# Kernel optimization log

Hardware: AMD Instinct MI355X
Metric: run time of the kernel (lower is better)

## Reference

```python
import jax, jax.numpy as jnp
import numpy as np
from jax.scipy.special import logsumexp

EPS = 0.1
MAX_ITER = 10


def setup_inputs() -> dict:
    key = jax.random.key(0)
    kx, ky, kp, kq = jax.random.split(key, 4)
    N, M, D = 4096, 4096, 64
    x = jax.random.normal(kx, (N, D), dtype=jnp.float32)
    y = jax.random.normal(ky, (M, D), dtype=jnp.float32)
    p = jax.random.uniform(kp, (N,), dtype=jnp.float32, minval=0.1, maxval=1.0)
    q = jax.random.uniform(kq, (M,), dtype=jnp.float32, minval=0.1, maxval=1.0)
    p = p / p.sum()  # valid probability marginals (log(p) is taken)
    q = q / q.sum()
    return {"x": x, "y": y, "p": p, "q": q}


def _cost_matrix(x, y):
    # squared L2 cost: C[i,j] = ||x_i - y_j||^2, shape [N, M]
    return jnp.sum((x[:, None, :] - y[None, :, :]) ** 2, axis=-1)


def _S(C, f, g):
    # eq. 4.43/4.44 log-domain kernel: (-C + f_i + g_j) / eps
    return (-C + f[:, None] + g[None, :]) / EPS


def _sinkhorn(C, p, q):
    logp = jnp.log(p)
    logq = jnp.log(q)
    f0 = jnp.zeros_like(p)
    g0 = jnpep = jnp.zeros_like(q)

    def step(carry, _):
        f, g = carry
        f = f + EPS * (logp - logsumexp(_S(C, f, g), axis=-1))   # row reduce
        g = g + EPS * (logq - logsumexp(_S(C, f, g), axis=0))    # col reduce (== .T row reduce)
        return (f, g), None

    (f, g), _ = jax.lax.scan(step, (f0, jnp.zeros_like(q)), None, length=MAX_ITER)
    P = jnp.exp(_S(C, f, g))
    w_cost = jnp.sum(P * C)
    return w_cost, P


def reference(x, y, p, q):
    C = _cost_matrix(x, y)
    return _sinkhorn(C, p, q)
```

## Files before the change

### kernel.cpp

```cpp
#include <hip/hip_runtime.h>
#include <hip/hip_bf16.h>
#include <cstdint>
#include <cstddef>

#define NROW 4096
#define NM ((size_t)NROW * (size_t)NROW)

#define SCONST 14.426950408889634f
#define EPS_LN2 0.0693147180559945f
#define ENC 461.66241308446827f
#define DEC 0.0625f
#define NEGBIG -3.0e38f

#if __has_builtin(__builtin_amdgcn_exp2f)
#define FEXP2(x) __builtin_amdgcn_exp2f(x)
#else
#define FEXP2(x) exp2f(x)
#endif
#if __has_builtin(__builtin_amdgcn_logf)
#define FLOG2(x) __builtin_amdgcn_logf(x)
#else
#define FLOG2(x) log2f(x)
#endif

__global__ void init_kernel(const float* __restrict__ x, const float* __restrict__ y,
                            const float* __restrict__ p, const float* __restrict__ q,
                            float* __restrict__ lp, float* __restrict__ lq,
                            float* __restrict__ a,
                            float* __restrict__ xn, float* __restrict__ yn) {
    int t = blockIdx.x * blockDim.x + threadIdx.x;
    if (t >= NROW) return;
    lp[t] = FLOG2(p[t]);
    lq[t] = FLOG2(q[t]);
    const float* xr = x + (size_t)t * 64;
    const float* yr = y + (size_t)t * 64;
    float sx = 0.f, sy = 0.f;
    #pragma unroll
    for (int d = 0; d < 64; ++d) {
        sx = fmaf(xr[d], xr[d], sx);
        sy = fmaf(yr[d], yr[d], sy);
    }
    xn[t] = sx; yn[t] = sy;
    a[t] = -SCONST * sy;
}

__global__ __launch_bounds__(256) void M16_kernel(const float* __restrict__ x,
                                                  const float* __restrict__ y,
                                                  int16_t* __restrict__ M16) {
    __shared__ float xs[64 * 65];
    __shared__ float ys[64 * 65];
    int tid = threadIdx.x;
    int it = blockIdx.y, jt = blockIdx.x;
    for (int k = tid; k < 4096; k += 256) {
        int r = k >> 6, d = k & 63;
        xs[r * 65 + d] = x[(size_t)it * 4096 + k];
        ys[r * 65 + d] = y[(size_t)jt * 4096 + k];
    }
    __syncthreads();
    int rl = tid >> 4;
    int cl = tid & 15;
    float acc[4][4] = {};
    #pragma unroll 8
    for (int d = 0; d < 64; ++d) {
        float xv[4], yv[4];
        #pragma unroll
        for (int i = 0; i < 4; ++i) xv[i] = xs[(rl + 16 * i) * 65 + d];
        #pragma unroll
        for (int j = 0; j < 4; ++j) yv[j] = ys[(cl * 4 + j) * 65 + d];
        #pragma unroll
        for (int i = 0; i < 4; ++i)
            #pragma unroll
            for (int j = 0; j < 4; ++j)
                acc[i][j] = fmaf(xv[i], yv[j], acc[i][j]);
    }
    #pragma unroll
    for (int i = 0; i < 4; ++i) {
        int row = it * 64 + rl + 16 * i;
        short4 o;
        short* op = (short*)&o;
        #pragma unroll
        for (int j = 0; j < 4; ++j) {
            float e = __builtin_rintf(ENC * acc[i][j]);
            e = fmaxf(-32767.f, fminf(32767.f, e));
            op[j] = (short)(int)e;
        }
        *(short4*)(M16 + (size_t)row * 4096 + jt * 64 + cl * 4) = o;
    }
}

__global__ __launch_bounds__(256) void pass16_row(const int16_t* __restrict__ M16,
                                                  const float* __restrict__ ain,
                                                  const float* __restrict__ lp,
                                                  float* __restrict__ bt) {
    int tid = threadIdx.x;
    int lane = tid & 63, w = tid >> 6;
    int i0 = blockIdx.x * 4;
    const int4* r0 = (const int4*)(M16 + (size_t)i0 * 4096);
    float m[4] = {NEGBIG, NEGBIG, NEGBIG, NEGBIG};
    float s[4] = {0.f, 0.f, 0.f, 0.f};
    #pragma unroll
    for (int k = 0; k < 2; ++k) {
        int idx8 = tid + 256 * k;
        float4 a0 = *(const float4*)(ain + 8 * idx8);
        float4 a1 = *(const float4*)(ain + 8 * idx8 + 4);
        int4 v[4];
        v[0] = r0[idx8];
        v[1] = r0[idx8 + 512];
        v[2] = r0[idx8 + 1024];
        v[3] = r0[idx8 + 1536];
        #pragma unroll
        for (int r = 0; r < 4; ++r) {
            float u0 = fmaf(DEC, (float)(short)(v[r].x), a0.x);
            float u1 = fmaf(DEC, (float)(v[r].x >> 16),  a0.y);
            float u2 = fmaf(DEC, (float)(short)(v[r].y), a0.z);
            float u3 = fmaf(DEC, (float)(v[r].y >> 16),  a0.w);
            float u4 = fmaf(DEC, (float)(short)(v[r].z), a1.x);
            float u5 = fmaf(DEC, (float)(v[r].z >> 16),  a1.y);
            float u6 = fmaf(DEC, (float)(short)(v[r].w), a1.z);
            float u7 = fmaf(DEC, (float)(v[r].w >> 16),  a1.w);
            float mA = fmaxf(fmaxf(u0, u1), fmaxf(u2, u3));
            float mB = fmaxf(fmaxf(u4, u5), fmaxf(u6, u7));
            float nm = fmaxf(m[r], fmaxf(mA, mB));
            float e = ((FEXP2(u0 - nm) + FEXP2(u1 - nm)) + (FEXP2(u2 - nm) + FEXP2(u3 - nm)))
                    + ((FEXP2(u4 - nm) + FEXP2(u5 - nm)) + (FEXP2(u6 - nm) + FEXP2(u7 - nm)));
            s[r] = fmaf(s[r], FEXP2(m[r] - nm), e);
            m[r] = nm;
        }
    }
    __shared__ float sm[4][4];
    __shared__ float ss[4][4];
    #pragma unroll
    for (int r = 0; r < 4; ++r) {
        float mr = m[r], sr = s[r];
        #pragma unroll
        for (int off = 32; off >= 1; off >>= 1) {
            float om = __shfl_xor(mr, off);
            float os = __shfl_xor(sr, off);
            float nm = fmaxf(mr, om);
            sr = fmaf(sr, FEXP2(mr - nm), os * FEXP2(om - nm));
            mr = nm;
        }
        if (lane == 0) { sm[w][r] = mr; ss[w][r] = sr; }
    }
    __syncthreads();
    if (tid < 4) {
        float m0 = sm[0][tid], s0 = ss[0][tid];
        #pragma unroll
        for (int w2 = 1; w2 < 4; ++w2) {
            float m1 = sm[w2][tid], s1 = ss[w2][tid];
            float nm = fmaxf(m0, m1);
            s0 = fmaf(s0, FEXP2(m0 - nm), s1 * FEXP2(m1 - nm));
            m0 = nm;
        }
        int i = i0 + tid;
        bt[i] = lp[i] - (m0 + FLOG2(s0));
    }
}

__global__ __launch_bounds__(256) void pass16_col(const int16_t* __restrict__ M16,
                                                  const float* __restrict__ bt,
                                                  float* __restrict__ Lpart) {
    int tid = threadIdx.x;
    int lane = tid & 63, w = tid >> 6;
    int col0 = blockIdx.x * 256 + lane * 4;
    int row0 = blockIdx.y * 128 + w * 32;
    float mc[4] = {NEGBIG, NEGBIG, NEGBIG, NEGBIG};
    float sc[4] = {0.f, 0.f, 0.f, 0.f};
    #pragma unroll 4
    for (int r = 0; r < 32; ++r) {
        int row = row0 + r;
        float b = bt[row];
        int2 v = *(const int2*)(M16 + (size_t)row * 4096 + col0);
        float e0 = fmaf(DEC, (float)(short)(v.x), b);
        float e1 = fmaf(DEC, (float)(v.x >> 16),  b);
        float e2 = fmaf(DEC, (float)(short)(v.y), b);
        float e3 = fmaf(DEC, (float)(v.y >> 16),  b);
        float e[4] = {e0, e1, e2, e3};
        #pragma unroll
        for (int c = 0; c < 4; ++c) {
            float nm = fmaxf(mc[c], e[c]);
            sc[c] = fmaf(sc[c], FEXP2(mc[c] - nm), FEXP2(e[c] - nm));
            mc[c] = nm;
        }
    }
    __shared__ float lm[4][256];
    __shared__ float ls[4][256];
    #pragma unroll
    for (int c = 0; c < 4; ++c) {
        lm[w][lane * 4 + c] = mc[c];
        ls[w][lane * 4 + c] = sc[c];
    }
    __syncthreads();
    float m0 = lm[0][tid], s0 = ls[0][tid];
    #pragma unroll
    for (int w2 = 1; w2 < 4; ++w2) {
        float m1 = lm[w2][tid], s1 = ls[w2][tid];
        float nm = fmaxf(m0, m1);
        s0 = fmaf(s0, FEXP2(m0 - nm), s1 * FEXP2(m1 - nm));
        m0 = nm;
    }
    Lpart[(size_t)blockIdx.y * 4096 + blockIdx.x * 256 + tid] = m0 + FLOG2(s0);
}

__global__ __launch_bounds__(256) void colcombine16(const float* __restrict__ Lpart,
                                                    const float* __restrict__ lq,
                                                    float* __restrict__ aout) {
    int j = blockIdx.x * 256 + threadIdx.x;
    float v[32];
    #pragma unroll
    for (int g = 0; g < 32; ++g) v[g] = Lpart[(size_t)g * 4096 + j];
    float m[4], s[4];
    #pragma unroll
    for (int t = 0; t < 4; ++t) { m[t] = NEGBIG; s[t] = 0.f; }
    #pragma unroll
    for (int g = 0; g < 32; ++g) {
        int t = g & 3;
        float nm = fmaxf(m[t], v[g]);
        s[t] = fmaf(s[t], FEXP2(m[t] - nm), FEXP2(v[g] - nm));
        m[t] = nm;
    }
    float mm = m[0], ss = s[0];
    #pragma unroll
    for (int t = 1; t < 4; ++t) {
        float nm = fmaxf(mm, m[t]);
        ss = fmaf(ss, FEXP2(mm - nm), s[t] * FEXP2(m[t] - nm));
        mm = nm;
    }
    aout[j] = lq[j] - (mm + FLOG2(ss));
}

__global__ __launch_bounds__(256) void pcost16(const int16_t* __restrict__ M16,
                                               const float* __restrict__ a,
                                               const float* __restrict__ yn,
                                               const float* __restrict__ bt,
                                               const float* __restrict__ xn,
                                               float* __restrict__ P,
                                               float* __restrict__ part) {
    int tid = threadIdx.x;
    int i = blockIdx.x;
    float bi = bt[i];
    float xni = xn[i];
    const int4* Mrow = (const int4*)(M16 + (size_t)i * 4096);
    float* Prow = P + (size_t)i * 4096;
    float acc = 0.f;
    #pragma unroll
    for (int k = 0; k < 2; ++k) {
        int idx8 = tid + 256 * k;
        int4 v = Mrow[idx8];
        float mv[8];
        mv[0] = DEC * (float)(short)(v.x); mv[1] = DEC * (float)(v.x >> 16);
        mv[2] = DEC * (float)(short)(v.y); mv[3] = DEC * (float)(v.y >> 16);
        mv[4] = DEC * (float)(short)(v.z); mv[5] = DEC * (float)(v.z >> 16);
        mv[6] = DEC * (float)(short)(v.w); mv[7] = DEC * (float)(v.w >> 16);
        float4 a0 = *(const float4*)(a + 8 * idx8);
        float4 a1 = *(const float4*)(a + 8 * idx8 + 4);
        float4 y0 = *(const float4*)(yn + 8 * idx8);
        float4 y1 = *(const float4*)(yn + 8 * idx8 + 4);
        float av[8] = {a0.x, a0.y, a0.z, a0.w, a1.x, a1.y, a1.z, a1.w};
        float yv[8] = {y0.x, y0.y, y0.z, y0.w, y1.x, y1.y, y1.z, y1.w};
        #pragma unroll
        for (int e = 0; e < 8; ++e) {
            float Pv = FEXP2(bi + av[e] + mv[e]);
            float Cv = xni + yv[e] - EPS_LN2 * mv[e];
            Prow[8 * idx8 + e] = Pv;
            acc = fmaf(Pv, Cv, acc);
        }
    }
    #pragma unroll
    for (int off = 32; off >= 1; off >>= 1) acc += __shfl_xor(acc, off);
    __shared__ float sw[4];
    if ((tid & 63) == 0) sw[tid >> 6] = acc;
    __syncthreads();
    if (tid == 0) part[blockIdx.x] = (sw[0] + sw[1]) + (sw[2] + sw[3]);
}

__global__ __launch_bounds__(256) void reduce_kernel(const float* __restrict__ part,
                                                     float* __restrict__ out0) {
    int tid = threadIdx.x;
    float acc = 0.f;
    #pragma unroll
    for (int k = 0; k < 16; ++k) acc += part[tid + 256 * k];
    #pragma unroll
    for (int off = 32; off >= 1; off >>= 1) acc += __shfl_xor(acc, off);
    __shared__ float sw[4];
    if ((tid & 63) == 0) sw[tid >> 6] = acc;
    __syncthreads();
    if (tid == 0) out0[0] = (sw[0] + sw[1]) + (sw[2] + sw[3]);
}

extern "C" void kernel_launch(void* const* d_in, const int* in_sizes, int n_in,
                              void* d_out, int out_size, void* d_ws, size_t ws_size,
                              hipStream_t stream) {
    const float* x = (const float*)d_in[0];
    const float* y = (const float*)d_in[1];
    const float* p = (const float*)d_in[2];
    const float* q = (const float*)d_in[3];
    float* out = (float*)d_out;
    char* ws = (char*)d_ws;

    float* lp    = (float*)(ws + 0 * 16384);
    float* lq    = (float*)(ws + 1 * 16384);
    float* a     = (float*)(ws + 2 * 16384);
    float* bt    = (float*)(ws + 3 * 16384);
    float* xn    = (float*)(ws + 4 * 16384);
    float* yn    = (float*)(ws + 5 * 16384);
    float* part  = (float*)(ws + 6 * 16384);
    float* Lpart = (float*)(ws + (1 << 20));
    int16_t* M16 = (int16_t*)(ws + (16u << 20));

    init_kernel<<<16, 256, 0, stream>>>(x, y, p, q, lp, lq, a, xn, yn);
    M16_kernel<<<dim3(64, 64), 256, 0, stream>>>(x, y, M16);

    for (int iter = 0; iter < 10; ++iter) {
        pass16_row<<<1024, 256, 0, stream>>>(M16, a, lp, bt);
        pass16_col<<<dim3(16, 32), 256, 0, stream>>>(M16, bt, Lpart);
        colcombine16<<<16, 256, 0, stream>>>(Lpart, lq, a);
    }

    pcost16<<<4096, 256, 0, stream>>>(M16, a, yn, bt, xn, out + 1, part);
    reduce_kernel<<<1, 256, 0, stream>>>(part, out);
}
```

Baseline: 270.7 us.

## Fuse row and column Sinkhorn passes using previous column LSE as stabilizer; MFMA cost matrix

Iterations after the first now run a single pass over the int16 cost matrix. Each pass computes the row log-sum-exp and accumulates column partial sums, using the previous iteration's column LSE as the max shift, and a small kernel combines the partials. This halves matrix reads per iteration. The cost-matrix build also moves to bf16 MFMA with hi/lo splitting for near-fp32 accuracy. The risk is overflow or underflow if the column shift drifts far from the true maximum between iterations.

```diff
diff --git a/kernel.cpp b/kernel.cpp
--- a/kernel.cpp
+++ b/kernel.cpp
@@ -22,6 +22,19 @@
 #else
 #define FLOG2(x) log2f(x)
 #endif
+
+using frag16 = __attribute__((ext_vector_type(8))) short;
+using f32x4v = __attribute__((ext_vector_type(4))) float;
+
+__device__ __forceinline__ unsigned short f2bf_rne(float f) {
+    unsigned u = __builtin_bit_cast(unsigned, f);
+    unsigned r = (u + 0x7fffu + ((u >> 16) & 1u)) >> 16;
+    return (unsigned short)r;
+}
+__device__ __forceinline__ float bf2f(unsigned short h) {
+    unsigned u = ((unsigned)h) << 16;
+    return __builtin_bit_cast(float, u);
+}
 
 __global__ void init_kernel(const float* __restrict__ x, const float* __restrict__ y,
                             const float* __restrict__ p, const float* __restrict__ q,
@@ -44,47 +57,75 @@
     a[t] = -SCONST * sy;
 }
 
-__global__ __launch_bounds__(256) void M16_kernel(const float* __restrict__ x,
-                                                  const float* __restrict__ y,
-                                                  int16_t* __restrict__ M16) {
-    __shared__ float xs[64 * 65];
-    __shared__ float ys[64 * 65];
-    int tid = threadIdx.x;
+__global__ __launch_bounds__(256) void M16_mfma(const float* __restrict__ x,
+                                                const float* __restrict__ y,
+                                                int16_t* __restrict__ M16) {
+    int tid = threadIdx.x;
+    int lane = tid & 63;
+    int wid = tid >> 6;
     int it = blockIdx.y, jt = blockIdx.x;
-    for (int k = tid; k < 4096; k += 256) {
-        int r = k >> 6, d = k & 63;
-        xs[r * 65 + d] = x[(size_t)it * 4096 + k];
-        ys[r * 65 + d] = y[(size_t)jt * 4096 + k];
-    }
-    __syncthreads();
-    int rl = tid >> 4;
-    int cl = tid & 15;
-    float acc[4][4] = {};
-    #pragma unroll 8
-    for (int d = 0; d < 64; ++d) {
-        float xv[4], yv[4];
-        #pragma unroll
-        for (int i = 0; i < 4; ++i) xv[i] = xs[(rl + 16 * i) * 65 + d];
-        #pragma unroll
-        for (int j = 0; j < 4; ++j) yv[j] = ys[(cl * 4 + j) * 65 + d];
-        #pragma unroll
-        for (int i = 0; i < 4; ++i)
+    int rowbase = it * 128 + (wid >> 1) * 64;
+    int colbase = jt * 128 + (wid & 1) * 64;
+    int l15 = lane & 15;
+    int kseg = lane >> 4;
+
+    f32x4v acc[4][4];
+    #pragma unroll
+    for (int i = 0; i < 4; ++i)
+        #pragma unroll
+        for (int j = 0; j < 4; ++j)
+            acc[i][j] = (f32x4v){0.f, 0.f, 0.f, 0.f};
+
+    #pragma unroll
+    for (int kk = 0; kk < 2; ++kk) {
+        frag16 bhi[4], blo[4];
+        #pragma unroll
+        for (int ct = 0; ct < 4; ++ct) {
+            const float* src = y + (size_t)(colbase + ct * 16 + l15) * 64 + kk * 32 + kseg * 8;
+            float4 f0 = *(const float4*)src;
+            float4 f1 = *(const float4*)(src + 4);
+            float f[8] = {f0.x, f0.y, f0.z, f0.w, f1.x, f1.y, f1.z, f1.w};
             #pragma unroll
-            for (int j = 0; j < 4; ++j)
-                acc[i][j] = fmaf(xv[i], yv[j], acc[i][j]);
-    }
-    #pragma unroll
-    for (int i = 0; i < 4; ++i) {
-        int row = it * 64 + rl + 16 * i;
-        short4 o;
-        short* op = (short*)&o;
-        #pragma unroll
-        for (int j = 0; j < 4; ++j) {
-            float e = __builtin_rintf(ENC * acc[i][j]);
-            e = fmaxf(-32767.f, fminf(32767.f, e));
-            op[j] = (short)(int)e;
-        }
-        *(short4*)(M16 + (size_t)row * 4096 + jt * 64 + cl * 4) = o;
+            for (int e = 0; e < 8; ++e) {
+                unsigned short h = f2bf_rne(f[e]);
+                bhi[ct][e] = (short)h;
+                blo[ct][e] = (short)f2bf_rne(f[e] - bf2f(h));
+            }
+        }
+        #pragma unroll
+        for (int rt = 0; rt < 4; ++rt) {
+            const float* src = x + (size_t)(rowbase + rt * 16 + l15) * 64 + kk * 32 + kseg * 8;
+            float4 f0 = *(const float4*)src;
+            float4 f1 = *(const float4*)(src + 4);
+            float f[8] = {f0.x, f0.y, f0.z, f0.w, f1.x, f1.y, f1.z, f1.w};
+            frag16 ahi, alo;
+            #pragma unroll
+            for (int e = 0; e < 8; ++e) {
+                unsigned short h = f2bf_rne(f[e]);
+                ahi[e] = (short)h;
+                alo[e] = (short)f2bf_rne(f[e] - bf2f(h));
+            }
+            #pragma unroll
+            for (int ct = 0; ct < 4; ++ct) {
+                acc[rt][ct] = __builtin_amdgcn_mfma_f32_16x16x32_bf16(ahi, bhi[ct], acc[rt][ct], 0, 0, 0);
+                acc[rt][ct] = __builtin_amdgcn_mfma_f32_16x16x32_bf16(ahi, blo[ct], acc[rt][ct], 0, 0, 0);
+                acc[rt][ct] = __builtin_amdgcn_mfma_f32_16x16x32_bf16(alo, bhi[ct], acc[rt][ct], 0, 0, 0);
+            }
+        }
+    }
+    #pragma unroll
+    for (int rt = 0; rt < 4; ++rt) {
+        #pragma unroll
+        for (int ct = 0; ct < 4; ++ct) {
+            #pragma unroll
+            for (int r = 0; r < 4; ++r) {
+                int row = rowbase + rt * 16 + (lane >> 4) * 4 + r;
+                int col = colbase + ct * 16 + l15;
+                float e = __builtin_rintf(ENC * acc[rt][ct][r]);
+                e = fmaxf(-32767.f, fminf(32767.f, e));
+                M16[(size_t)row * 4096 + col] = (int16_t)(int)e;
+            }
+        }
     }
 }
 
@@ -204,7 +245,8 @@
 
 __global__ __launch_bounds__(256) void colcombine16(const float* __restrict__ Lpart,
                                                     const float* __restrict__ lq,
-                                                    float* __restrict__ aout) {
+                                                    float* __restrict__ aout,
+                                                    float* __restrict__ Lout) {
     int j = blockIdx.x * 256 + threadIdx.x;
     float v[32];
     #pragma unroll
@@ -226,7 +268,132 @@
         ss = fmaf(ss, FEXP2(mm - nm), s[t] * FEXP2(m[t] - nm));
         mm = nm;
     }
-    aout[j] = lq[j] - (mm + FLOG2(ss));
+    float L = mm + FLOG2(ss);
+    aout[j] = lq[j] - L;
+    Lout[j] = L;
+}
+
+__global__ __launch_bounds__(256) void pass_fused(const int16_t* __restrict__ M16,
+                                                  const float* __restrict__ ain,
+                                                  const float* __restrict__ lp,
+                                                  const float* __restrict__ Lprev,
+                                                  float* __restrict__ bt,
+                                                  float* __restrict__ spart) {
+    __shared__ float smm[8][4];
+    __shared__ float sss[8][4];
+    int tid = threadIdx.x;
+    int lane = tid & 63, w = tid >> 6;
+    int row0 = blockIdx.x * 8;
+
+    float av[16], mP[16], sc[16];
+    #pragma unroll
+    for (int k = 0; k < 2; ++k) {
+        int base = 8 * (tid + 256 * k);
+        float4 a0 = *(const float4*)(ain + base);
+        float4 a1 = *(const float4*)(ain + base + 4);
+        float4 p0 = *(const float4*)(Lprev + base);
+        float4 p1 = *(const float4*)(Lprev + base + 4);
+        av[8 * k + 0] = a0.x; av[8 * k + 1] = a0.y; av[8 * k + 2] = a0.z; av[8 * k + 3] = a0.w;
+        av[8 * k + 4] = a1.x; av[8 * k + 5] = a1.y; av[8 * k + 6] = a1.z; av[8 * k + 7] = a1.w;
+        mP[8 * k + 0] = p0.x; mP[8 * k + 1] = p0.y; mP[8 * k + 2] = p0.z; mP[8 * k + 3] = p0.w;
+        mP[8 * k + 4] = p1.x; mP[8 * k + 5] = p1.y; mP[8 * k + 6] = p1.z; mP[8 * k + 7] = p1.w;
+    }
+    #pragma unroll
+    for (int c = 0; c < 16; ++c) sc[c] = 0.f;
+
+    for (int r = 0; r < 8; ++r) {
+        int row = row0 + r;
+        const int4* Mr = (const int4*)(M16 + ((size_t)row << 12));
+        int4 v0 = Mr[tid];
+        int4 v1 = Mr[tid + 256];
+        float mv[16];
+        mv[0]  = DEC * (float)(short)(v0.x); mv[1]  = DEC * (float)(v0.x >> 16);
+        mv[2]  = DEC * (float)(short)(v0.y); mv[3]  = DEC * (float)(v0.y >> 16);
+        mv[4]  = DEC * (float)(short)(v0.z); mv[5]  = DEC * (float)(v0.z >> 16);
+        mv[6]  = DEC * (float)(short)(v0.w); mv[7]  = DEC * (float)(v0.w >> 16);
+        mv[8]  = DEC * (float)(short)(v1.x); mv[9]  = DEC * (float)(v1.x >> 16);
+        mv[10] = DEC * (float)(short)(v1.y); mv[11] = DEC * (float)(v1.y >> 16);
+        mv[12] = DEC * (float)(short)(v1.z); mv[13] = DEC * (float)(v1.z >> 16);
+        mv[14] = DEC * (float)(short)(v1.w); mv[15] = DEC * (float)(v1.w >> 16);
+        float u[16];
+        #pragma unroll
+        for (int c = 0; c < 16; ++c) u[c] = av[c] + mv[c];
+        float mA = fmaxf(fmaxf(fmaxf(u[0], u[1]), fmaxf(u[2], u[3])),
+                         fmaxf(fmaxf(u[4], u[5]), fmaxf(u[6], u[7])));
+        float mB = fmaxf(fmaxf(fmaxf(u[8], u[9]), fmaxf(u[10], u[11])),
+                         fmaxf(fmaxf(u[12], u[13]), fmaxf(u[14], u[15])));
+        float m = fmaxf(mA, mB);
+        float s = 0.f;
+        #pragma unroll
+        for (int c = 0; c < 16; ++c) s += FEXP2(u[c] - m);
+        #pragma unroll
+        for (int off = 32; off >= 1; off >>= 1) {
+            float om = __shfl_xor(m, off);
+            float os = __shfl_xor(s, off);
+            float nm = fmaxf(m, om);
+            s = fmaf(s, FEXP2(m - nm), os * FEXP2(om - nm));
+            m = nm;
+        }
+        if (lane == 0) { smm[r][w] = m; sss[r][w] = s; }
+        __syncthreads();
+        float M0 = smm[r][0], S0 = sss[r][0];
+        #pragma unroll
+        for (int w2 = 1; w2 < 4; ++w2) {
+            float M1 = smm[r][w2], S1 = sss[r][w2];
+            float nm = fmaxf(M0, M1);
+            S0 = fmaf(S0, FEXP2(M0 - nm), S1 * FEXP2(M1 - nm));
+            M0 = nm;
+        }
+        float b = lp[row] - (M0 + FLOG2(S0));
+        if (tid == r) bt[row] = b;
+        #pragma unroll
+        for (int c = 0; c < 16; ++c)
+            sc[c] += FEXP2((b - mP[c]) + mv[c]);
+    }
+    float* sp = spart + ((size_t)blockIdx.x << 12);
+    #pragma unroll
+    for (int k = 0; k < 2; ++k) {
+        int base = 8 * (tid + 256 * k);
+        float4 o0 = make_float4(sc[8 * k + 0], sc[8 * k + 1], sc[8 * k + 2], sc[8 * k + 3]);
+        float4 o1 = make_float4(sc[8 * k + 4], sc[8 * k + 5], sc[8 * k + 6], sc[8 * k + 7]);
+        *(float4*)(sp + base) = o0;
+        *(float4*)(sp + base + 4) = o1;
+    }
+}
+
+__global__ __launch_bounds__(256) void combine_fused(const float* __restrict__ spart,
+                                                     const float* __restrict__ lq,
+                                                     float* __restrict__ aout,
+                                                     float* __restrict__ Lcol) {
+    __shared__ float smw[4][8];
+    int tid = threadIdx.x;
+    int lane = tid & 63, w = tid >> 6;
+    int g = blockIdx.x;
+    const float* p0 = spart + (size_t)tid * 4096 + 8 * g;
+    const float* p1 = spart + (size_t)(tid + 256) * 4096 + 8 * g;
+    float4 A0 = *(const float4*)p0;
+    float4 A1 = *(const float4*)(p0 + 4);
+    float4 B0 = *(const float4*)p1;
+    float4 B1 = *(const float4*)(p1 + 4);
+    float v[8] = {A0.x + B0.x, A0.y + B0.y, A0.z + B0.z, A0.w + B0.w,
+                  A1.x + B1.x, A1.y + B1.y, A1.z + B1.z, A1.w + B1.w};
+    #pragma unroll
+    for (int off = 32; off >= 1; off >>= 1) {
+        #pragma unroll
+        for (int j = 0; j < 8; ++j) v[j] += __shfl_xor(v[j], off);
+    }
+    if (lane == 0) {
+        #pragma unroll
+        for (int j = 0; j < 8; ++j) smw[w][j] = v[j];
+    }
+    __syncthreads();
+    if (tid < 8) {
+        float s = (smw[0][tid] + smw[1][tid]) + (smw[2][tid] + smw[3][tid]);
+        int col = 8 * g + tid;
+        float L = Lcol[col] + FLOG2(s);
+        aout[col] = lq[col] - L;
+        Lcol[col] = L;
+    }
 }
 
 __global__ __launch_bounds__(256) void pcost16(const int16_t* __restrict__ M16,
@@ -305,16 +472,21 @@
     float* xn    = (float*)(ws + 4 * 16384);
     float* yn    = (float*)(ws + 5 * 16384);
     float* part  = (float*)(ws + 6 * 16384);
+    float* Lcol  = (float*)(ws + 7 * 16384);
     float* Lpart = (float*)(ws + (1 << 20));
+    float* spart = (float*)(ws + (2u << 20));
     int16_t* M16 = (int16_t*)(ws + (16u << 20));
 
     init_kernel<<<16, 256, 0, stream>>>(x, y, p, q, lp, lq, a, xn, yn);
-    M16_kernel<<<dim3(64, 64), 256, 0, stream>>>(x, y, M16);
-
-    for (int iter = 0; iter < 10; ++iter) {
-        pass16_row<<<1024, 256, 0, stream>>>(M16, a, lp, bt);
-        pass16_col<<<dim3(16, 32), 256, 0, stream>>>(M16, bt, Lpart);
-        colcombine16<<<16, 256, 0, stream>>>(Lpart, lq, a);
+    M16_mfma<<<dim3(32, 32), 256, 0, stream>>>(x, y, M16);
+
+    pass16_row<<<1024, 256, 0, stream>>>(M16, a, lp, bt);
+    pass16_col<<<dim3(16, 32), 256, 0, stream>>>(M16, bt, Lpart);
+    colcombine16<<<16, 256, 0, stream>>>(Lpart, lq, a, Lcol);
+
+    for (int iter = 1; iter < 10; ++iter) {
+        pass_fused<<<512, 256, 0, stream>>>(M16, a, lp, Lcol, bt, spart);
+        combine_fused<<<512, 256, 0, stream>>>(spart, lq, a, Lcol);
     }
 
     pcost16<<<4096, 256, 0, stream>>>(M16, a, yn, bt, xn, out + 1, part);
```

Measured after the change: 314.4 us. +16.2%, slower.

## Compute cost matrix with split-bf16 MFMA and fuse column combine via last-block atomics

Applied to the files above, without the earlier changes.

The cost-matrix kernel is rewritten to use bf16 MFMA instructions, with a three-term hi/lo split that approximates fp32 accuracy. Results are staged through shared memory so the int16 output is written with coalesced stores. The per-iteration column combine kernel is folded into the column pass: an atomic counter per stripe lets the last finishing block do the final log-sum-exp merge, removing ten kernel launches. This adds a memset, atomics and fences, and the split-bf16 product may differ slightly from the exact fp32 result.

```diff
diff --git a/kernel.cpp b/kernel.cpp
--- a/kernel.cpp
+++ b/kernel.cpp
@@ -22,6 +22,19 @@
 #else
 #define FLOG2(x) log2f(x)
 #endif
+
+using frag16 = __attribute__((ext_vector_type(8))) short;
+using f32x4v = __attribute__((ext_vector_type(4))) float;
+
+__device__ __forceinline__ unsigned short f2bf_rne(float f) {
+    unsigned u = __builtin_bit_cast(unsigned, f);
+    unsigned r = (u + 0x7fffu + ((u >> 16) & 1u)) >> 16;
+    return (unsigned short)r;
+}
+__device__ __forceinline__ float bf2f(unsigned short h) {
+    unsigned u = ((unsigned)h) << 16;
+    return __builtin_bit_cast(float, u);
+}
 
 __global__ void init_kernel(const float* __restrict__ x, const float* __restrict__ y,
                             const float* __restrict__ p, const float* __restrict__ q,
@@ -44,47 +57,87 @@
     a[t] = -SCONST * sy;
 }
 
-__global__ __launch_bounds__(256) void M16_kernel(const float* __restrict__ x,
-                                                  const float* __restrict__ y,
-                                                  int16_t* __restrict__ M16) {
-    __shared__ float xs[64 * 65];
-    __shared__ float ys[64 * 65];
-    int tid = threadIdx.x;
+__global__ __launch_bounds__(256) void M16_mfma(const float* __restrict__ x,
+                                                const float* __restrict__ y,
+                                                int16_t* __restrict__ M16) {
+    __shared__ int16_t tile[128][136];
+    int tid = threadIdx.x;
+    int lane = tid & 63;
+    int wid = tid >> 6;
     int it = blockIdx.y, jt = blockIdx.x;
-    for (int k = tid; k < 4096; k += 256) {
-        int r = k >> 6, d = k & 63;
-        xs[r * 65 + d] = x[(size_t)it * 4096 + k];
-        ys[r * 65 + d] = y[(size_t)jt * 4096 + k];
-    }
-    __syncthreads();
-    int rl = tid >> 4;
-    int cl = tid & 15;
-    float acc[4][4] = {};
-    #pragma unroll 8
-    for (int d = 0; d < 64; ++d) {
-        float xv[4], yv[4];
-        #pragma unroll
-        for (int i = 0; i < 4; ++i) xv[i] = xs[(rl + 16 * i) * 65 + d];
-        #pragma unroll
-        for (int j = 0; j < 4; ++j) yv[j] = ys[(cl * 4 + j) * 65 + d];
-        #pragma unroll
-        for (int i = 0; i < 4; ++i)
+    int rloc = (wid >> 1) * 64;
+    int cloc = (wid & 1) * 64;
+    int l15 = lane & 15;
+    int g4  = lane >> 4;
+
+    f32x4v acc[4][4];
+    #pragma unroll
+    for (int i = 0; i < 4; ++i)
+        #pragma unroll
+        for (int j = 0; j < 4; ++j)
+            acc[i][j] = (f32x4v){0.f, 0.f, 0.f, 0.f};
+
+    #pragma unroll
+    for (int kk = 0; kk < 2; ++kk) {
+        frag16 yhi[4], ylo[4];
+        #pragma unroll
+        for (int ct = 0; ct < 4; ++ct) {
+            const float* src = y + (size_t)(jt * 128 + cloc + ct * 16 + l15) * 64 + kk * 32 + g4 * 8;
+            float4 f0 = *(const float4*)src;
+            float4 f1 = *(const float4*)(src + 4);
+            float f[8] = {f0.x, f0.y, f0.z, f0.w, f1.x, f1.y, f1.z, f1.w};
             #pragma unroll
-            for (int j = 0; j < 4; ++j)
-                acc[i][j] = fmaf(xv[i], yv[j], acc[i][j]);
-    }
-    #pragma unroll
-    for (int i = 0; i < 4; ++i) {
-        int row = it * 64 + rl + 16 * i;
-        short4 o;
-        short* op = (short*)&o;
-        #pragma unroll
-        for (int j = 0; j < 4; ++j) {
-            float e = __builtin_rintf(ENC * acc[i][j]);
-            e = fmaxf(-32767.f, fminf(32767.f, e));
-            op[j] = (short)(int)e;
-        }
-        *(short4*)(M16 + (size_t)row * 4096 + jt * 64 + cl * 4) = o;
+            for (int e = 0; e < 8; ++e) {
+                unsigned short h = f2bf_rne(f[e]);
+                yhi[ct][e] = (short)h;
+                ylo[ct][e] = (short)f2bf_rne(f[e] - bf2f(h));
+            }
+        }
+        #pragma unroll
+        for (int rt = 0; rt < 4; ++rt) {
+            const float* src = x + (size_t)(it * 128 + rloc + rt * 16 + l15) * 64 + kk * 32 + g4 * 8;
+            float4 f0 = *(const float4*)src;
+            float4 f1 = *(const float4*)(src + 4);
+            float f[8] = {f0.x, f0.y, f0.z, f0.w, f1.x, f1.y, f1.z, f1.w};
+            frag16 xhi, xlo;
+            #pragma unroll
+            for (int e = 0; e < 8; ++e) {
+                unsigned short h = f2bf_rne(f[e]);
+                xhi[e] = (short)h;
+                xlo[e] = (short)f2bf_rne(f[e] - bf2f(h));
+            }
+            #pragma unroll
+            for (int ct = 0; ct < 4; ++ct) {
+                acc[rt][ct] = __builtin_amdgcn_mfma_f32_16x16x32_bf16(yhi[ct], xhi, acc[rt][ct], 0, 0, 0);
+                acc[rt][ct] = __builtin_amdgcn_mfma_f32_16x16x32_bf16(ylo[ct], xhi, acc[rt][ct], 0, 0, 0);
+                acc[rt][ct] = __builtin_amdgcn_mfma_f32_16x16x32_bf16(yhi[ct], xlo, acc[rt][ct], 0, 0, 0);
+            }
+        }
+    }
+    #pragma unroll
+    for (int rt = 0; rt < 4; ++rt) {
+        int row = rloc + rt * 16 + l15;
+        #pragma unroll
+        for (int ct = 0; ct < 4; ++ct) {
+            int col = cloc + ct * 16 + g4 * 4;
+            short4 o;
+            short* op = (short*)&o;
+            #pragma unroll
+            for (int r = 0; r < 4; ++r) {
+                float e = __builtin_rintf(ENC * acc[rt][ct][r]);
+                e = fmaxf(-32767.f, fminf(32767.f, e));
+                op[r] = (short)(int)e;
+            }
+            *(short4*)&tile[row][col] = o;
+        }
+    }
+    __syncthreads();
+    #pragma unroll
+    for (int pass = 0; pass < 8; ++pass) {
+        int row = (tid >> 4) + 16 * pass;
+        int c16 = (tid & 15) * 8;
+        int4 v = *(const int4*)&tile[row][c16];
+        *(int4*)(M16 + (size_t)(it * 128 + row) * 4096 + jt * 128 + c16) = v;
     }
 }
 
@@ -157,12 +210,16 @@
     }
 }
 
-__global__ __launch_bounds__(256) void pass16_col(const int16_t* __restrict__ M16,
-                                                  const float* __restrict__ bt,
-                                                  float* __restrict__ Lpart) {
+__global__ __launch_bounds__(256) void pass16_colC(const int16_t* __restrict__ M16,
+                                                   const float* __restrict__ bt,
+                                                   const float* __restrict__ lq,
+                                                   float* __restrict__ Lpart,
+                                                   float* __restrict__ aout,
+                                                   int* __restrict__ cnt) {
     int tid = threadIdx.x;
     int lane = tid & 63, w = tid >> 6;
-    int col0 = blockIdx.x * 256 + lane * 4;
+    int stripe = blockIdx.x;
+    int col0 = stripe * 256 + lane * 4;
     int row0 = blockIdx.y * 128 + w * 32;
     float mc[4] = {NEGBIG, NEGBIG, NEGBIG, NEGBIG};
     float sc[4] = {0.f, 0.f, 0.f, 0.f};
@@ -199,34 +256,40 @@
         s0 = fmaf(s0, FEXP2(m0 - nm), s1 * FEXP2(m1 - nm));
         m0 = nm;
     }
-    Lpart[(size_t)blockIdx.y * 4096 + blockIdx.x * 256 + tid] = m0 + FLOG2(s0);
-}
-
-__global__ __launch_bounds__(256) void colcombine16(const float* __restrict__ Lpart,
-                                                    const float* __restrict__ lq,
-                                                    float* __restrict__ aout) {
-    int j = blockIdx.x * 256 + threadIdx.x;
-    float v[32];
-    #pragma unroll
-    for (int g = 0; g < 32; ++g) v[g] = Lpart[(size_t)g * 4096 + j];
-    float m[4], s[4];
-    #pragma unroll
-    for (int t = 0; t < 4; ++t) { m[t] = NEGBIG; s[t] = 0.f; }
+    Lpart[(size_t)blockIdx.y * 4096 + stripe * 256 + tid] = m0 + FLOG2(s0);
+
+    __threadfence();
+    __shared__ int lastFlag;
+    if (tid == 0) {
+        int old = atomicAdd(&cnt[stripe], 1);
+        lastFlag = (old == 31);
+    }
+    __syncthreads();
+    if (!lastFlag) return;
+    __threadfence();
+
+    int j = stripe * 256 + tid;
+    float vv[32];
+    #pragma unroll
+    for (int g = 0; g < 32; ++g) vv[g] = Lpart[(size_t)g * 4096 + j];
+    float m4[4], s4[4];
+    #pragma unroll
+    for (int t = 0; t < 4; ++t) { m4[t] = NEGBIG; s4[t] = 0.f; }
     #pragma unroll
     for (int g = 0; g < 32; ++g) {
         int t = g & 3;
-        float nm = fmaxf(m[t], v[g]);
-        s[t] = fmaf(s[t], FEXP2(m[t] - nm), FEXP2(v[g] - nm));
-        m[t] = nm;
-    }
-    float mm = m[0], ss = s[0];
+        float nm = fmaxf(m4[t], vv[g]);
+        s4[t] = fmaf(s4[t], FEXP2(m4[t] - nm), FEXP2(vv[g] - nm));
+        m4[t] = nm;
+    }
+    float mm = m4[0], ssx = s4[0];
     #pragma unroll
     for (int t = 1; t < 4; ++t) {
-        float nm = fmaxf(mm, m[t]);
-        ss = fmaf(ss, FEXP2(mm - nm), s[t] * FEXP2(m[t] - nm));
+        float nm = fmaxf(mm, m4[t]);
+        ssx = fmaf(ssx, FEXP2(mm - nm), s4[t] * FEXP2(m4[t] - nm));
         mm = nm;
     }
-    aout[j] = lq[j] - (mm + FLOG2(ss));
+    aout[j] = lq[j] - (mm + FLOG2(ssx));
 }
 
 __global__ __launch_bounds__(256) void pcost16(const int16_t* __restrict__ M16,
@@ -305,16 +368,17 @@
     float* xn    = (float*)(ws + 4 * 16384);
     float* yn    = (float*)(ws + 5 * 16384);
     float* part  = (float*)(ws + 6 * 16384);
+    int*   cnt   = (int*)  (ws + 7 * 16384);
     float* Lpart = (float*)(ws + (1 << 20));
     int16_t* M16 = (int16_t*)(ws + (16u << 20));
 
+    hipMemsetAsync(cnt, 0, 160 * sizeof(int), stream);
     init_kernel<<<16, 256, 0, stream>>>(x, y, p, q, lp, lq, a, xn, yn);
-    M16_kernel<<<dim3(64, 64), 256, 0, stream>>>(x, y, M16);
+    M16_mfma<<<dim3(32, 32), 256, 0, stream>>>(x, y, M16);
 
     for (int iter = 0; iter < 10; ++iter) {
         pass16_row<<<1024, 256, 0, stream>>>(M16, a, lp, bt);
-        pass16_col<<<dim3(16, 32), 256, 0, stream>>>(M16, bt, Lpart);
-        colcombine16<<<16, 256, 0, stream>>>(Lpart, lq, a);
+        pass16_colC<<<dim3(16, 32), 256, 0, stream>>>(M16, bt, lq, Lpart, a, cnt + iter * 16);
     }
 
     pcost16<<<4096, 256, 0, stream>>>(M16, a, yn, bt, xn, out + 1, part);
```

Result: slower. 594.1 us (+119.5%).
